# Performance work log

Measured on AMD Instinct MI355X. Metric: run time of the kernel, lower is better.

Reference implementation:

```python
import jax, jax.numpy as jnp
import numpy as np

B = 131072
D = 64
NUM_REL = 32


def setup_inputs() -> dict:
    key = jax.random.key(0)
    k1, k2, k3, k4 = jax.random.split(key, 4)
    embeds1 = jax.random.normal(k1, (B, D), dtype=jnp.float32)
    embeds2 = jax.random.normal(k2, (B, D), dtype=jnp.float32)
    rels = jax.random.randint(k3, (B,), 0, NUM_REL, dtype=jnp.int32)
    # learned relation table: one D*D matrix per relation type
    rel_embeds = jax.random.normal(k4, (NUM_REL, D * D), dtype=jnp.float32)
    return {"embeds1": embeds1, "embeds2": embeds2, "rels": rels,
            "rel_embeds": rel_embeds}


def reference(embeds1, embeds2, rels, rel_embeds):
    # gather per-sample relation matrices: [B, D, D]
    rel_mats = rel_embeds[rels].reshape(-1, D, D)
    # per-sample bilinear form: score_b = e1_b^T R_b e2_b  -> [B]
    e1R = jnp.einsum("bd,bde->be", embeds1, rel_mats)
    return (e1R * embeds2).sum(axis=1)
```

## Files before the change

kernel.cpp:

```cpp
#include <hip/hip_runtime.h>
#include <hip/hip_bf16.h>
#include <cstddef>

#define BB 131072
#define DD 64
#define NREL 32
#define PADN 133120
#define NWAVE (PADN / 64)

#define BLOCKS_AC 512
#define SPB (BB / BLOCKS_AC)
#define CHUNKS 8
#define BPC (BLOCKS_AC / CHUNKS)

typedef __attribute__((ext_vector_type(8))) __bf16 bf16x8;
typedef __attribute__((ext_vector_type(16))) float f32x16;

__global__ __launch_bounds__(256) void phaseA_hist(
    const int* __restrict__ rels, int* __restrict__ blockCnt,
    int* __restrict__ permPacked) {
  __shared__ int hist[NREL];
  const int t = threadIdx.x;
  if (t < NREL) hist[t] = 0;
  __syncthreads();
  const int gid = blockIdx.x * 256 + t;
  permPacked[gid] = -1;
  if (gid < PADN - BB) permPacked[BB + gid] = -1;
  atomicAdd(&hist[rels[gid]], 1);
  __syncthreads();
  if (t < NREL) blockCnt[blockIdx.x * NREL + t] = hist[t];
}

__global__ __launch_bounds__(256) void phaseB_scan(
    const int* __restrict__ blockCnt, int* __restrict__ blockOff,
    int* __restrict__ binBase) {
  __shared__ int partial[CHUNKS][NREL];
  __shared__ int chunkBase[CHUNKS][NREL];
  __shared__ int binB[NREL];
  const int t = threadIdx.x;
  const int c = t >> 5;
  const int r = t & 31;
  const int b0 = c * BPC;
  int run = 0;
#pragma unroll 4
  for (int b = 0; b < BPC; ++b) run += blockCnt[(b0 + b) * NREL + r];
  partial[c][r] = run;
  __syncthreads();
  if (t < NREL) {
    int acc = 0;
#pragma unroll
    for (int i = 0; i < CHUNKS; ++i) { chunkBase[i][t] = acc; acc += partial[i][t]; }
  }
  __syncthreads();
  if (t == 0) {
    int acc = 0;
#pragma unroll
    for (int i = 0; i < NREL; ++i) {
      binB[i] = acc;
      const int tot = chunkBase[CHUNKS - 1][i] + partial[CHUNKS - 1][i];
      acc += (tot + 63) & ~63;
    }
  }
  __syncthreads();
  if (t < NREL) binBase[t] = binB[t];
  int run2 = chunkBase[c][r];
#pragma unroll 4
  for (int b = 0; b < BPC; ++b) {
    blockOff[(b0 + b) * NREL + r] = run2;
    run2 += blockCnt[(b0 + b) * NREL + r];
  }
}

__global__ __launch_bounds__(256) void phaseC_scatter(
    const int* __restrict__ rels, const int* __restrict__ blockOff,
    const int* __restrict__ binBase, int* __restrict__ permPacked) {
  __shared__ int cnt[NREL];
  __shared__ int baseArr[NREL];
  const int t = threadIdx.x;
  if (t < NREL) {
    cnt[t] = 0;
    baseArr[t] = binBase[t] + blockOff[blockIdx.x * NREL + t];
  }
  __syncthreads();
  const int s = blockIdx.x * SPB + t;
  const int rv = rels[s];
  const int rank = atomicAdd(&cnt[rv], 1);
  permPacked[baseArr[rv] + rank] = (rv << 17) | s;
}

__global__ __launch_bounds__(64) void bilinear_mfma(
    const float* __restrict__ e1g, const float* __restrict__ e2g,
    const float* __restrict__ relE, const int* __restrict__ permPacked,
    float* __restrict__ out) {
  __shared__ float sP[64 * 33];
  const int lane = threadIdx.x;
  const int pk = permPacked[blockIdx.x * 64 + lane];
  const unsigned long long vm = __ballot(pk >= 0);
  if (vm == 0ull) return;
  const int fv = (int)__builtin_ctzll(vm);
  const int r0 = __builtin_amdgcn_readlane(pk, fv) >> 17;
  const int h = lane >> 5;
  const int l31 = lane & 31;
  const int rowid0 = __shfl(pk, l31) & 0x1FFFF;
  const int rowid1 = __shfl(pk, 32 + l31) & 0x1FFFF;

  const float* __restrict__ R = relE + (size_t)r0 * (DD * DD);

  f32x16 acc[2][2];
#pragma unroll
  for (int ti = 0; ti < 2; ++ti)
#pragma unroll
    for (int tj = 0; tj < 2; ++tj)
#pragma unroll
      for (int i = 0; i < 16; ++i) acc[ti][tj][i] = 0.f;

#pragma unroll
  for (int kc = 0; kc < 4; ++kc) {
    bf16x8 aH[2], aL[2], bH[2], bL[2];
#pragma unroll
    for (int ti = 0; ti < 2; ++ti) {
      const float* ap =
          e1g + (size_t)(ti ? rowid1 : rowid0) * DD + kc * 16 + 8 * h;
      const float4 x0 = *(const float4*)(ap);
      const float4 x1 = *(const float4*)(ap + 4);
      const float xs[8] = {x0.x, x0.y, x0.z, x0.w, x1.x, x1.y, x1.z, x1.w};
#pragma unroll
      for (int j = 0; j < 8; ++j) {
        const __bf16 hb = (__bf16)xs[j];
        aH[ti][j] = hb;
        aL[ti][j] = (__bf16)(xs[j] - (float)hb);
      }
    }
#pragma unroll
    for (int tj = 0; tj < 2; ++tj) {
      const float* q = R + (size_t)(kc * 16 + 8 * h) * DD + 32 * tj + l31;
#pragma unroll
      for (int j = 0; j < 8; ++j) {
        const float x = q[(size_t)j * DD];
        const __bf16 hb = (__bf16)x;
        bH[tj][j] = hb;
        bL[tj][j] = (__bf16)(x - (float)hb);
      }
    }
#pragma unroll
    for (int ti = 0; ti < 2; ++ti)
#pragma unroll
      for (int tj = 0; tj < 2; ++tj) {
        acc[ti][tj] = __builtin_amdgcn_mfma_f32_32x32x16_bf16(aH[ti], bH[tj], acc[ti][tj], 0, 0, 0);
        acc[ti][tj] = __builtin_amdgcn_mfma_f32_32x32x16_bf16(aH[ti], bL[tj], acc[ti][tj], 0, 0, 0);
        acc[ti][tj] = __builtin_amdgcn_mfma_f32_32x32x16_bf16(aL[ti], bH[tj], acc[ti][tj], 0, 0, 0);
      }
  }

#pragma unroll
  for (int ti = 0; ti < 2; ++ti)
#pragma unroll
    for (int g = 0; g < 4; ++g)
#pragma unroll
      for (int q = 0; q < 4; ++q) {
        const int reg = g * 4 + q;
        const int rbase = 32 * ti + q + 8 * g;
        const int s0 = __builtin_amdgcn_readlane(pk, rbase) & 0x1FFFF;
        const int s1 = __builtin_amdgcn_readlane(pk, rbase + 4) & 0x1FFFF;
        const int bs = h ? s1 : s0;
        const float* er = e2g + (size_t)bs * DD + l31;
        const float v = fmaf(acc[ti][0][reg], er[0], acc[ti][1][reg] * er[32]);
        sP[(rbase + 4 * h) * 33 + l31] = v;
      }
  __syncthreads();
  float sc = 0.f;
#pragma unroll
  for (int c = 0; c < 32; ++c) sc += sP[lane * 33 + c];
  if (pk >= 0) out[pk & 0x1FFFF] = sc;
}

extern "C" void kernel_launch(void* const* d_in, const int* in_sizes, int n_in,
                              void* d_out, int out_size, void* d_ws, size_t ws_size,
                              hipStream_t stream) {
  const float* e1 = (const float*)d_in[0];
  const float* e2 = (const float*)d_in[1];
  const int* rels = (const int*)d_in[2];
  const float* relE = (const float*)d_in[3];
  float* out = (float*)d_out;

  int* permPacked = (int*)d_ws;
  int* blockCnt = permPacked + PADN;
  int* blockOff = blockCnt + BLOCKS_AC * NREL;
  int* binBase = blockOff + BLOCKS_AC * NREL;

  phaseA_hist<<<BLOCKS_AC, 256, 0, stream>>>(rels, blockCnt, permPacked);
  phaseB_scan<<<1, 256, 0, stream>>>(blockCnt, blockOff, binBase);
  phaseC_scatter<<<BLOCKS_AC, 256, 0, stream>>>(rels, blockOff, binBase, permPacked);
  bilinear_mfma<<<NWAVE, 64, 0, stream>>>(e1, e2, relE, permPacked, out);
}
```

Measured before the change: 113.5 us.

## Fuse single-block scan into scatter kernel with redundant per-block prefix

Removes the single-block scan launch. Each scatter block now rereads the full 512x32 block-count table and computes its own exclusive prefix and bin bases before scattering. This drops one kernel launch and a serial single-block stage, at the cost of every block redundantly reading the 64KB count table.

```diff
diff --git a/kernel.cpp b/kernel.cpp
--- a/kernel.cpp
+++ b/kernel.cpp
@@ -9,7 +9,6 @@
 #define NWAVE (PADN / 64)
 
 #define BLOCKS_AC 512
-#define SPB (BB / BLOCKS_AC)
 #define CHUNKS 8
 #define BPC (BLOCKS_AC / CHUNKS)
 
@@ -31,61 +30,49 @@
   if (t < NREL) blockCnt[blockIdx.x * NREL + t] = hist[t];
 }
 
-__global__ __launch_bounds__(256) void phaseB_scan(
-    const int* __restrict__ blockCnt, int* __restrict__ blockOff,
-    int* __restrict__ binBase) {
-  __shared__ int partial[CHUNKS][NREL];
-  __shared__ int chunkBase[CHUNKS][NREL];
-  __shared__ int binB[NREL];
+__global__ __launch_bounds__(256) void scatter_scan(
+    const int* __restrict__ rels, const int* __restrict__ blockCnt,
+    int* __restrict__ permPacked) {
+  __shared__ int sF[CHUNKS][NREL];
+  __shared__ int sPp[CHUNKS][NREL];
+  __shared__ int sTot[NREL];
+  __shared__ int sS[NREL];
+  __shared__ int sBase[NREL];
+  __shared__ int cnt[NREL];
   const int t = threadIdx.x;
+  const int b = blockIdx.x;
   const int c = t >> 5;
   const int r = t & 31;
   const int b0 = c * BPC;
-  int run = 0;
+  int F = 0, Pp = 0;
 #pragma unroll 4
-  for (int b = 0; b < BPC; ++b) run += blockCnt[(b0 + b) * NREL + r];
-  partial[c][r] = run;
+  for (int i = 0; i < BPC; ++i) {
+    const int v = blockCnt[(b0 + i) * NREL + r];
+    F += v;
+    if (b0 + i < b) Pp += v;
+  }
+  sF[c][r] = F;
+  sPp[c][r] = Pp;
+  if (t < NREL) cnt[t] = 0;
   __syncthreads();
   if (t < NREL) {
-    int acc = 0;
+    int S = 0, T = 0;
 #pragma unroll
-    for (int i = 0; i < CHUNKS; ++i) { chunkBase[i][t] = acc; acc += partial[i][t]; }
+    for (int c2 = 0; c2 < CHUNKS; ++c2) { S += sPp[c2][t]; T += sF[c2][t]; }
+    sS[t] = S;
+    sTot[t] = T;
   }
   __syncthreads();
-  if (t == 0) {
-    int acc = 0;
-#pragma unroll
-    for (int i = 0; i < NREL; ++i) {
-      binB[i] = acc;
-      const int tot = chunkBase[CHUNKS - 1][i] + partial[CHUNKS - 1][i];
-      acc += (tot + 63) & ~63;
-    }
+  if (t < NREL) {
+    int bb = 0;
+    for (int r2 = 0; r2 < t; ++r2) bb += (sTot[r2] + 63) & ~63;
+    sBase[t] = bb;
   }
   __syncthreads();
-  if (t < NREL) binBase[t] = binB[t];
-  int run2 = chunkBase[c][r];
-#pragma unroll 4
-  for (int b = 0; b < BPC; ++b) {
-    blockOff[(b0 + b) * NREL + r] = run2;
-    run2 += blockCnt[(b0 + b) * NREL + r];
-  }
-}
-
-__global__ __launch_bounds__(256) void phaseC_scatter(
-    const int* __restrict__ rels, const int* __restrict__ blockOff,
-    const int* __restrict__ binBase, int* __restrict__ permPacked) {
-  __shared__ int cnt[NREL];
-  __shared__ int baseArr[NREL];
-  const int t = threadIdx.x;
-  if (t < NREL) {
-    cnt[t] = 0;
-    baseArr[t] = binBase[t] + blockOff[blockIdx.x * NREL + t];
-  }
-  __syncthreads();
-  const int s = blockIdx.x * SPB + t;
+  const int s = b * 256 + t;
   const int rv = rels[s];
   const int rank = atomicAdd(&cnt[rv], 1);
-  permPacked[baseArr[rv] + rank] = (rv << 17) | s;
+  permPacked[sBase[rv] + sS[rv] + rank] = (rv << 17) | s;
 }
 
 __global__ __launch_bounds__(64) void bilinear_mfma(
@@ -185,11 +172,8 @@
 
   int* permPacked = (int*)d_ws;
   int* blockCnt = permPacked + PADN;
-  int* blockOff = blockCnt + BLOCKS_AC * NREL;
-  int* binBase = blockOff + BLOCKS_AC * NREL;
 
   phaseA_hist<<<BLOCKS_AC, 256, 0, stream>>>(rels, blockCnt, permPacked);
-  phaseB_scan<<<1, 256, 0, stream>>>(blockCnt, blockOff, binBase);
-  phaseC_scatter<<<BLOCKS_AC, 256, 0, stream>>>(rels, blockOff, binBase, permPacked);
+  scatter_scan<<<BLOCKS_AC, 256, 0, stream>>>(rels, blockCnt, permPacked);
   bilinear_mfma<<<NWAVE, 64, 0, stream>>>(e1, e2, relE, permPacked, out);
 }
```

Measured after the change: 110.6 us. -2.6%, faster.
